# Performance work log

Hardware: AMD Instinct MI355X
Metric: run time of the kernel (lower is better)

The kernel has to match this reference:

```python
import jax, jax.numpy as jnp
import numpy as np

# Blade metric for Cl(1,3) inner product <~A B>_0: sign per basis blade =
# (-1)^{k(k-1)/2} * prod(eta_ii) with eta = diag(1,-1,-1,-1).
# Order: 1 | e0 e1 e2 e3 | e01 e02 e03 e12 e13 e23 | e012 e013 e023 e123 | e0123
BLADE_METRIC = jnp.array(
    [1.0,
     1.0, -1.0, -1.0, -1.0,
     1.0, 1.0, 1.0, -1.0, -1.0, -1.0,
     -1.0, -1.0, -1.0, 1.0,
     -1.0],
    dtype=jnp.float32,
)

B, H, N, MVC, SC = 8, 8, 1024, 8, 32


def setup_inputs() -> dict:
    key = jax.random.key(0)
    ks = jax.random.split(key, 6)
    mv_shape = (B, H, N, MVC, 16)
    s_shape = (B, H, N, SC)
    return {
        "q_mv": jax.random.normal(ks[0], mv_shape, dtype=jnp.float32),
        "k_mv": jax.random.normal(ks[1], mv_shape, dtype=jnp.float32),
        "v_mv": jax.random.normal(ks[2], mv_shape, dtype=jnp.float32),
        "q_s": jax.random.normal(ks[3], s_shape, dtype=jnp.float32),
        "k_s": jax.random.normal(ks[4], s_shape, dtype=jnp.float32),
        "v_s": jax.random.normal(ks[5], s_shape, dtype=jnp.float32),
    }


def reference(q_mv, k_mv, v_mv, q_s, k_s, v_s):
    *lead, n_out, mvc, _ = q_mv.shape
    n_in = k_mv.shape[-3]
    sc = q_s.shape[-1]
    d = 16 * mvc + sc  # total feature dim used for the softmax scale

    # Apply GA blade metric to queries, flatten mv channels, concat scalars.
    qf = jnp.concatenate(
        [(q_mv * BLADE_METRIC).reshape(*lead, n_out, mvc * 16), q_s], axis=-1
    )
    kf = jnp.concatenate([k_mv.reshape(*lead, n_in, mvc * 16), k_s], axis=-1)
    vf = jnp.concatenate([v_mv.reshape(*lead, n_in, mvc * 16), v_s], axis=-1)

    scores = jnp.einsum("bhid,bhjd->bhij", qf, kf) / jnp.sqrt(
        jnp.asarray(d, dtype=qf.dtype)
    )
    attn = jax.nn.softmax(scores, axis=-1)
    out = jnp.einsum("bhij,bhjd->bhid", attn, vf)

    out_mv = out[..., : mvc * 16].reshape(*lead, n_out, mvc, 16)
    out_s = out[..., mvc * 16 :]
    return out_mv, out_s
```

## Files before the change

kernel.cpp:

```cpp
#include <hip/hip_runtime.h>

typedef __attribute__((ext_vector_type(8))) _Float16 f16x8;
typedef __attribute__((ext_vector_type(4))) _Float16 f16x4;
typedef __attribute__((ext_vector_type(4))) float f32x4;

#define BHn 64
#define Nn 1024

static constexpr int kOutMvElems = 8 * 8 * 1024 * 128;
static constexpr float kScaleLog2e = 0.11405506f;
static constexpr unsigned kNegMask = 0xBF1Cu;

__global__ __launch_bounds__(256) void pack_k_kernel(const float* __restrict__ kmv,
                                                     const float* __restrict__ ks,
                                                     _Float16* __restrict__ Kf) {
  int t = blockIdx.x * 256 + threadIdx.x;
  const int total = BHn * Nn * 20;
  if (t >= total) return;
  int row = t / 20, s = t - row * 20;
  const float* src = (s < 16) ? (kmv + (size_t)row * 128 + s * 8)
                              : (ks + (size_t)row * 32 + (s - 16) * 8);
  float4 a = *(const float4*)src;
  float4 b = *(const float4*)(src + 4);
  f16x8 h;
  h[0] = (_Float16)a.x; h[1] = (_Float16)a.y; h[2] = (_Float16)a.z; h[3] = (_Float16)a.w;
  h[4] = (_Float16)b.x; h[5] = (_Float16)b.y; h[6] = (_Float16)b.z; h[7] = (_Float16)b.w;
  *(f16x8*)(Kf + (size_t)row * 160 + s * 8) = h;
}

__global__ __launch_bounds__(256) void pack_vt_kernel(const float* __restrict__ vmv,
                                                      const float* __restrict__ vs,
                                                      _Float16* __restrict__ Vt) {
  __shared__ _Float16 tile[160][72];
  const int bh = blockIdx.y;
  const int kt = blockIdx.x;
  const int tid = threadIdx.x;
  for (int s = tid; s < 64 * 40; s += 256) {
    int key = s / 40, p = s - key * 40;
    int row = bh * Nn + kt * 64 + key;
    const float* src = (p < 32) ? (vmv + (size_t)row * 128 + p * 4)
                                : (vs + (size_t)row * 32 + (p - 32) * 4);
    float4 v = *(const float4*)src;
    int d = p * 4;
    tile[d + 0][key] = (_Float16)v.x;
    tile[d + 1][key] = (_Float16)v.y;
    tile[d + 2][key] = (_Float16)v.z;
    tile[d + 3][key] = (_Float16)v.w;
  }
  __syncthreads();
  for (int s = tid; s < 160 * 8; s += 256) {
    int d = s >> 3, o = s & 7;
    int c32 = (o >> 2) * 32;
    int g4 = (o & 3) * 4;
    f16x4 lo = *(const f16x4*)&tile[d][c32 + g4];
    f16x4 hi = *(const f16x4*)&tile[d][c32 + 16 + g4];
    f16x8 h;
    h[0] = lo[0]; h[1] = lo[1]; h[2] = lo[2]; h[3] = lo[3];
    h[4] = hi[0]; h[5] = hi[1]; h[6] = hi[2]; h[7] = hi[3];
    *(f16x8*)(Vt + ((size_t)(bh * 160 + d)) * 1024 + kt * 64 + o * 8) = h;
  }
}

__global__ __launch_bounds__(512, 2) void geo_attn_kernel(const float* __restrict__ qmv,
                                                          const float* __restrict__ qs,
                                                          const _Float16* __restrict__ Kf,
                                                          const _Float16* __restrict__ Vt,
                                                          float* __restrict__ out) {
  __shared__ _Float16 k_lds[2][64 * 192];
  __shared__ _Float16 v_lds[2][160 * 64];

  const int b = blockIdx.x;
  const int sw = (b & 7) * 32 + (b >> 3);
  const int qb = sw & 3;
  const int bh = sw >> 2;

  const int tid = threadIdx.x;
  const int w = tid >> 6;
  const int l = tid & 63;
  const int g = l >> 4;
  const int nn = l & 15;
  const int swz = (nn & 7) << 3;

  f16x8 qf[2][5];
#pragma unroll
  for (int q2 = 0; q2 < 2; ++q2) {
    const size_t qbase = (size_t)(bh * Nn + qb * 256 + w * 32 + q2 * 16 + nn);
#pragma unroll
    for (int c = 0; c < 5; ++c) {
      const float* src = (c < 4) ? (qmv + qbase * 128 + c * 32 + 8 * g)
                                 : (qs + qbase * 32 + 8 * g);
      float4 a = *(const float4*)src;
      float4 bb = *(const float4*)(src + 4);
      float x[8] = {a.x, a.y, a.z, a.w, bb.x, bb.y, bb.z, bb.w};
#pragma unroll
      for (int i = 0; i < 8; ++i) {
        float v = x[i] * kScaleLog2e;
        if (c < 4) {
          int idx = ((g & 1) << 3) + i;
          v = ((kNegMask >> idx) & 1u) ? -v : v;
        }
        qf[q2][c][i] = (_Float16)v;
      }
    }
  }

  f32x4 acc[2][10];
#pragma unroll
  for (int q2 = 0; q2 < 2; ++q2)
#pragma unroll
    for (int j = 0; j < 10; ++j) acc[q2][j] = (f32x4){0.f, 0.f, 0.f, 0.f};
  float Ma = -3.0e38f, Mb = -3.0e38f, La = 0.f, Lb = 0.f;

  const _Float16* kgbase = Kf + (size_t)(bh * Nn) * 160;
  const _Float16* vgbase = Vt + (size_t)bh * 160 * Nn;

  f16x8 st[5];
  auto stage_load = [&](int key0) {
#pragma unroll
    for (int i = 0; i < 5; ++i) {
      int s = tid + 512 * i;
      if (s < 1280) {
        st[i] = *(const f16x8*)(kgbase + (size_t)key0 * 160 + s * 8);
      } else {
        int s2 = s - 1280;
        int d = s2 >> 3, cs = s2 & 7;
        st[i] = *(const f16x8*)(vgbase + (size_t)d * Nn + key0 + cs * 8);
      }
    }
  };
  auto stage_write = [&](int buf) {
#pragma unroll
    for (int i = 0; i < 5; ++i) {
      int s = tid + 512 * i;
      if (s < 1280) {
        int key = s / 20, p = s - key * 20;
        int idx = (key * 192 + p * 8) ^ ((key & 7) << 3);
        *(f16x8*)&k_lds[buf][idx] = st[i];
      } else {
        int s2 = s - 1280;
        int d = s2 >> 3, cs = s2 & 7;
        int idx = (d * 64 + cs * 8) ^ ((d & 7) << 3);
        *(f16x8*)&v_lds[buf][idx] = st[i];
      }
    }
  };

  stage_load(0);
  stage_write(0);
  __syncthreads();

  for (int it = 0; it < 16; ++it) {
    const int cur = it & 1;
    if (it < 15) stage_load((it + 1) * 64);

    f32x4 sa[4], sb[4];
#pragma unroll
    for (int kb = 0; kb < 4; ++kb) {
      sa[kb] = (f32x4){0.f, 0.f, 0.f, 0.f};
      sb[kb] = (f32x4){0.f, 0.f, 0.f, 0.f};
    }
    __builtin_amdgcn_s_setprio(1);
#pragma unroll
    for (int c = 0; c < 5; ++c) {
      f16x8 kf[4];
#pragma unroll
      for (int kb = 0; kb < 4; ++kb)
        kf[kb] = *(const f16x8*)&k_lds[cur][((16 * kb + nn) * 192 + c * 32 + 8 * g) ^ swz];
#pragma unroll
      for (int kb = 0; kb < 4; ++kb) {
        sa[kb] = __builtin_amdgcn_mfma_f32_16x16x32_f16(kf[kb], qf[0][c], sa[kb], 0, 0, 0);
        sb[kb] = __builtin_amdgcn_mfma_f32_16x16x32_f16(kf[kb], qf[1][c], sb[kb], 0, 0, 0);
      }
    }
    __builtin_amdgcn_s_setprio(0);

    float pma = fmaxf(fmaxf(fmaxf(fmaxf(sa[0][0], sa[0][1]), fmaxf(sa[0][2], sa[0][3])),
                            fmaxf(fmaxf(sa[1][0], sa[1][1]), fmaxf(sa[1][2], sa[1][3]))),
                      fmaxf(fmaxf(fmaxf(sa[2][0], sa[2][1]), fmaxf(sa[2][2], sa[2][3])),
                            fmaxf(fmaxf(sa[3][0], sa[3][1]), fmaxf(sa[3][2], sa[3][3]))));
    float pmb = fmaxf(fmaxf(fmaxf(fmaxf(sb[0][0], sb[0][1]), fmaxf(sb[0][2], sb[0][3])),
                            fmaxf(fmaxf(sb[1][0], sb[1][1]), fmaxf(sb[1][2], sb[1][3]))),
                      fmaxf(fmaxf(fmaxf(sb[2][0], sb[2][1]), fmaxf(sb[2][2], sb[2][3])),
                            fmaxf(fmaxf(sb[3][0], sb[3][1]), fmaxf(sb[3][2], sb[3][3]))));
    pma = fmaxf(pma, __shfl_xor(pma, 16));
    pma = fmaxf(pma, __shfl_xor(pma, 32));
    pmb = fmaxf(pmb, __shfl_xor(pmb, 16));
    pmb = fmaxf(pmb, __shfl_xor(pmb, 32));

    float fsa_l = 1.f, fsb_l = 1.f;
    bool defer = (pma - Ma <= 8.f) && (pmb - Mb <= 8.f);
    if (!__all((int)defer)) {
      float nMa = fmaxf(Ma, pma); fsa_l = exp2f(Ma - nMa); Ma = nMa;
      float nMb = fmaxf(Mb, pmb); fsb_l = exp2f(Mb - nMb); Mb = nMb;
      float fa[4], fb[4];
#pragma unroll
      for (int r = 0; r < 4; ++r) {
        fa[r] = __shfl(fsa_l, 4 * g + r, 16);
        fb[r] = __shfl(fsb_l, 4 * g + r, 16);
      }
#pragma unroll
      for (int j = 0; j < 10; ++j)
#pragma unroll
        for (int r = 0; r < 4; ++r) {
          acc[0][j][r] *= fa[r];
          acc[1][j][r] *= fb[r];
        }
    }

    float rsa = 0.f, rsb = 0.f;
    f16x8 paf[2], pbf[2];
#pragma unroll
    for (int kb = 0; kb < 4; ++kb) {
      const int ch = kb >> 1, off = (kb & 1) * 4;
#pragma unroll
      for (int r = 0; r < 4; ++r) {
        float pa_ = exp2f(sa[kb][r] - Ma);
        float pb_ = exp2f(sb[kb][r] - Mb);
        rsa += pa_; rsb += pb_;
        paf[ch][off + r] = (_Float16)pa_;
        pbf[ch][off + r] = (_Float16)pb_;
      }
    }
    rsa += __shfl_xor(rsa, 16); rsa += __shfl_xor(rsa, 32);
    rsb += __shfl_xor(rsb, 16); rsb += __shfl_xor(rsb, 32);
    La = La * fsa_l + rsa;
    Lb = Lb * fsb_l + rsb;

    __builtin_amdgcn_s_setprio(1);
#pragma unroll
    for (int ch = 0; ch < 2; ++ch) {
#pragma unroll
      for (int j = 0; j < 10; ++j) {
        f16x8 vb = *(const f16x8*)&v_lds[cur][((16 * j + nn) * 64 + ch * 32 + 8 * g) ^ swz];
        acc[0][j] = __builtin_amdgcn_mfma_f32_16x16x32_f16(paf[ch], vb, acc[0][j], 0, 0, 0);
        acc[1][j] = __builtin_amdgcn_mfma_f32_16x16x32_f16(pbf[ch], vb, acc[1][j], 0, 0, 0);
      }
    }
    __builtin_amdgcn_s_setprio(0);

    if (it < 15) stage_write(cur ^ 1);
    __syncthreads();
  }

  float ria = 1.f / La, rib = 1.f / Lb;
  float ra[4], rb_[4];
#pragma unroll
  for (int r = 0; r < 4; ++r) {
    ra[r] = __shfl(ria, 4 * g + r, 16);
    rb_[r] = __shfl(rib, 4 * g + r, 16);
  }
  const int row0 = bh * Nn + qb * 256 + w * 32;
#pragma unroll
  for (int j = 0; j < 10; ++j) {
    const int d = 16 * j + nn;
#pragma unroll
    for (int r = 0; r < 4; ++r) {
      float v0 = acc[0][j][r] * ra[r];
      float v1 = acc[1][j][r] * rb_[r];
      const int r0 = row0 + 4 * g + r;
      const int r1 = row0 + 16 + 4 * g + r;
      if (d < 128) {
        out[(size_t)r0 * 128 + d] = v0;
        out[(size_t)r1 * 128 + d] = v1;
      } else {
        out[(size_t)kOutMvElems + (size_t)r0 * 32 + (d - 128)] = v0;
        out[(size_t)kOutMvElems + (size_t)r1 * 32 + (d - 128)] = v1;
      }
    }
  }
}

extern "C" void kernel_launch(void* const* d_in, const int* in_sizes, int n_in,
                              void* d_out, int out_size, void* d_ws, size_t ws_size,
                              hipStream_t stream) {
  const float* qmv = (const float*)d_in[0];
  const float* kmv = (const float*)d_in[1];
  const float* vmv = (const float*)d_in[2];
  const float* qs = (const float*)d_in[3];
  const float* ks = (const float*)d_in[4];
  const float* vs = (const float*)d_in[5];
  float* out = (float*)d_out;

  _Float16* Kf = (_Float16*)d_ws;
  _Float16* Vt = Kf + (size_t)BHn * Nn * 160;

  pack_k_kernel<<<dim3((BHn * Nn * 20) / 256), dim3(256), 0, stream>>>(kmv, ks, Kf);
  pack_vt_kernel<<<dim3(16, BHn), dim3(256), 0, stream>>>(vmv, vs, Vt);
  geo_attn_kernel<<<dim3(256), dim3(512), 0, stream>>>(qmv, qs, Kf, Vt, out);
}
```

Measured before the change: 94.14 us.

## Use 256-thread blocks with single-buffered LDS and deferred row-sum reduction

Halves the block to 4 waves (128 query rows), doubles the grid to 512 blocks, and drops LDS double-buffering in favour of a single buffer behind two barriers per tile. The per-thread global and LDS staging offsets are precomputed once. The max cross-lane shuffle now runs only when a rescale is needed, and the row-sum shuffle reduction moves out of the loop to the end. The aim is more blocks per CU and fewer shuffles per iteration, at the cost of an extra barrier per tile and K/V being reloaded by twice as many blocks.

```diff
diff --git a/kernel.cpp b/kernel.cpp
--- a/kernel.cpp
+++ b/kernel.cpp
@@ -61,18 +61,18 @@
   }
 }
 
-__global__ __launch_bounds__(512, 2) void geo_attn_kernel(const float* __restrict__ qmv,
+__global__ __launch_bounds__(256, 2) void geo_attn_kernel(const float* __restrict__ qmv,
                                                           const float* __restrict__ qs,
                                                           const _Float16* __restrict__ Kf,
                                                           const _Float16* __restrict__ Vt,
                                                           float* __restrict__ out) {
-  __shared__ _Float16 k_lds[2][64 * 192];
-  __shared__ _Float16 v_lds[2][160 * 64];
+  __shared__ _Float16 k_lds[64 * 192];
+  __shared__ _Float16 v_lds[160 * 64];
 
   const int b = blockIdx.x;
-  const int sw = (b & 7) * 32 + (b >> 3);
-  const int qb = sw & 3;
-  const int bh = sw >> 2;
+  const int sw = (b & 7) * 64 + (b >> 3);
+  const int qb = sw & 7;
+  const int bh = sw >> 3;
 
   const int tid = threadIdx.x;
   const int w = tid >> 6;
@@ -81,10 +81,22 @@
   const int nn = l & 15;
   const int swz = (nn & 7) << 3;
 
+  int gK[5], lKi[5], gV[5], lVi[5];
+#pragma unroll
+  for (int i = 0; i < 5; ++i) {
+    int sk = tid + 256 * i;
+    int key = sk / 20, p = sk - key * 20;
+    gK[i] = key * 160 + p * 8;
+    lKi[i] = (key * 192 + p * 8) ^ ((key & 7) << 3);
+    int d = sk >> 3, cs = sk & 7;
+    gV[i] = d * Nn + cs * 8;
+    lVi[i] = (d * 64 + cs * 8) ^ ((d & 7) << 3);
+  }
+
   f16x8 qf[2][5];
 #pragma unroll
   for (int q2 = 0; q2 < 2; ++q2) {
-    const size_t qbase = (size_t)(bh * Nn + qb * 256 + w * 32 + q2 * 16 + nn);
+    const size_t qbase = (size_t)(bh * Nn + qb * 128 + w * 32 + q2 * 16 + nn);
 #pragma unroll
     for (int c = 0; c < 5; ++c) {
       const float* src = (c < 4) ? (qmv + qbase * 128 + c * 32 + 8 * g)
@@ -111,47 +123,28 @@
     for (int j = 0; j < 10; ++j) acc[q2][j] = (f32x4){0.f, 0.f, 0.f, 0.f};
   float Ma = -3.0e38f, Mb = -3.0e38f, La = 0.f, Lb = 0.f;
 
-  const _Float16* kgbase = Kf + (size_t)(bh * Nn) * 160;
-  const _Float16* vgbase = Vt + (size_t)bh * 160 * Nn;
-
-  f16x8 st[5];
-  auto stage_load = [&](int key0) {
-#pragma unroll
-    for (int i = 0; i < 5; ++i) {
-      int s = tid + 512 * i;
-      if (s < 1280) {
-        st[i] = *(const f16x8*)(kgbase + (size_t)key0 * 160 + s * 8);
-      } else {
-        int s2 = s - 1280;
-        int d = s2 >> 3, cs = s2 & 7;
-        st[i] = *(const f16x8*)(vgbase + (size_t)d * Nn + key0 + cs * 8);
-      }
-    }
-  };
-  auto stage_write = [&](int buf) {
-#pragma unroll
-    for (int i = 0; i < 5; ++i) {
-      int s = tid + 512 * i;
-      if (s < 1280) {
-        int key = s / 20, p = s - key * 20;
-        int idx = (key * 192 + p * 8) ^ ((key & 7) << 3);
-        *(f16x8*)&k_lds[buf][idx] = st[i];
-      } else {
-        int s2 = s - 1280;
-        int d = s2 >> 3, cs = s2 & 7;
-        int idx = (d * 64 + cs * 8) ^ ((d & 7) << 3);
-        *(f16x8*)&v_lds[buf][idx] = st[i];
-      }
-    }
-  };
-
-  stage_load(0);
-  stage_write(0);
+  const _Float16* kg = Kf + (size_t)(bh * Nn) * 160;
+  const _Float16* vg = Vt + (size_t)bh * 160 * Nn;
+
+  f16x8 st[10];
+#pragma unroll
+  for (int i = 0; i < 5; ++i) st[i] = *(const f16x8*)(kg + gK[i]);
+#pragma unroll
+  for (int i = 0; i < 5; ++i) st[5 + i] = *(const f16x8*)(vg + gV[i]);
+#pragma unroll
+  for (int i = 0; i < 5; ++i) *(f16x8*)&k_lds[lKi[i]] = st[i];
+#pragma unroll
+  for (int i = 0; i < 5; ++i) *(f16x8*)&v_lds[lVi[i]] = st[5 + i];
   __syncthreads();
 
   for (int it = 0; it < 16; ++it) {
-    const int cur = it & 1;
-    if (it < 15) stage_load((it + 1) * 64);
+    if (it < 15) {
+      const int key0 = (it + 1) * 64;
+#pragma unroll
+      for (int i = 0; i < 5; ++i) st[i] = *(const f16x8*)(kg + (size_t)key0 * 160 + gK[i]);
+#pragma unroll
+      for (int i = 0; i < 5; ++i) st[5 + i] = *(const f16x8*)(vg + key0 + gV[i]);
+    }
 
     f32x4 sa[4], sb[4];
 #pragma unroll
@@ -165,7 +158,7 @@
       f16x8 kf[4];
 #pragma unroll
       for (int kb = 0; kb < 4; ++kb)
-        kf[kb] = *(const f16x8*)&k_lds[cur][((16 * kb + nn) * 192 + c * 32 + 8 * g) ^ swz];
+        kf[kb] = *(const f16x8*)&k_lds[((16 * kb + nn) * 192 + c * 32 + 8 * g) ^ swz];
 #pragma unroll
       for (int kb = 0; kb < 4; ++kb) {
         sa[kb] = __builtin_amdgcn_mfma_f32_16x16x32_f16(kf[kb], qf[0][c], sa[kb], 0, 0, 0);
@@ -174,29 +167,28 @@
     }
     __builtin_amdgcn_s_setprio(0);
 
-    float pma = fmaxf(fmaxf(fmaxf(fmaxf(sa[0][0], sa[0][1]), fmaxf(sa[0][2], sa[0][3])),
+    float lma = fmaxf(fmaxf(fmaxf(fmaxf(sa[0][0], sa[0][1]), fmaxf(sa[0][2], sa[0][3])),
                             fmaxf(fmaxf(sa[1][0], sa[1][1]), fmaxf(sa[1][2], sa[1][3]))),
                       fmaxf(fmaxf(fmaxf(sa[2][0], sa[2][1]), fmaxf(sa[2][2], sa[2][3])),
                             fmaxf(fmaxf(sa[3][0], sa[3][1]), fmaxf(sa[3][2], sa[3][3]))));
-    float pmb = fmaxf(fmaxf(fmaxf(fmaxf(sb[0][0], sb[0][1]), fmaxf(sb[0][2], sb[0][3])),
+    float lmb = fmaxf(fmaxf(fmaxf(fmaxf(sb[0][0], sb[0][1]), fmaxf(sb[0][2], sb[0][3])),
                             fmaxf(fmaxf(sb[1][0], sb[1][1]), fmaxf(sb[1][2], sb[1][3]))),
                       fmaxf(fmaxf(fmaxf(sb[2][0], sb[2][1]), fmaxf(sb[2][2], sb[2][3])),
                             fmaxf(fmaxf(sb[3][0], sb[3][1]), fmaxf(sb[3][2], sb[3][3]))));
-    pma = fmaxf(pma, __shfl_xor(pma, 16));
-    pma = fmaxf(pma, __shfl_xor(pma, 32));
-    pmb = fmaxf(pmb, __shfl_xor(pmb, 16));
-    pmb = fmaxf(pmb, __shfl_xor(pmb, 32));
-
-    float fsa_l = 1.f, fsb_l = 1.f;
-    bool defer = (pma - Ma <= 8.f) && (pmb - Mb <= 8.f);
-    if (!__all((int)defer)) {
-      float nMa = fmaxf(Ma, pma); fsa_l = exp2f(Ma - nMa); Ma = nMa;
-      float nMb = fmaxf(Mb, pmb); fsb_l = exp2f(Mb - nMb); Mb = nMb;
+    bool need = (lma - Ma > 8.f) || (lmb - Mb > 8.f);
+    if (__any((int)need)) {
+      float pma = fmaxf(lma, __shfl_xor(lma, 16));
+      pma = fmaxf(pma, __shfl_xor(pma, 32));
+      float pmb = fmaxf(lmb, __shfl_xor(lmb, 16));
+      pmb = fmaxf(pmb, __shfl_xor(pmb, 32));
+      float nMa = fmaxf(Ma, pma); float fsa = exp2f(Ma - nMa); Ma = nMa;
+      float nMb = fmaxf(Mb, pmb); float fsb = exp2f(Mb - nMb); Mb = nMb;
+      La *= fsa; Lb *= fsb;
       float fa[4], fb[4];
 #pragma unroll
       for (int r = 0; r < 4; ++r) {
-        fa[r] = __shfl(fsa_l, 4 * g + r, 16);
-        fb[r] = __shfl(fsb_l, 4 * g + r, 16);
+        fa[r] = __shfl(fsa, 4 * g + r, 16);
+        fb[r] = __shfl(fsb, 4 * g + r, 16);
       }
 #pragma unroll
       for (int j = 0; j < 10; ++j)
@@ -221,27 +213,33 @@
         pbf[ch][off + r] = (_Float16)pb_;
       }
     }
-    rsa += __shfl_xor(rsa, 16); rsa += __shfl_xor(rsa, 32);
-    rsb += __shfl_xor(rsb, 16); rsb += __shfl_xor(rsb, 32);
-    La = La * fsa_l + rsa;
-    Lb = Lb * fsb_l + rsb;
+    La += rsa;
+    Lb += rsb;
 
     __builtin_amdgcn_s_setprio(1);
 #pragma unroll
     for (int ch = 0; ch < 2; ++ch) {
 #pragma unroll
       for (int j = 0; j < 10; ++j) {
-        f16x8 vb = *(const f16x8*)&v_lds[cur][((16 * j + nn) * 64 + ch * 32 + 8 * g) ^ swz];
+        f16x8 vb = *(const f16x8*)&v_lds[((16 * j + nn) * 64 + ch * 32 + 8 * g) ^ swz];
         acc[0][j] = __builtin_amdgcn_mfma_f32_16x16x32_f16(paf[ch], vb, acc[0][j], 0, 0, 0);
         acc[1][j] = __builtin_amdgcn_mfma_f32_16x16x32_f16(pbf[ch], vb, acc[1][j], 0, 0, 0);
       }
     }
     __builtin_amdgcn_s_setprio(0);
 
-    if (it < 15) stage_write(cur ^ 1);
-    __syncthreads();
-  }
-
+    if (it < 15) {
+      __syncthreads();
+#pragma unroll
+      for (int i = 0; i < 5; ++i) *(f16x8*)&k_lds[lKi[i]] = st[i];
+#pragma unroll
+      for (int i = 0; i < 5; ++i) *(f16x8*)&v_lds[lVi[i]] = st[5 + i];
+      __syncthreads();
+    }
+  }
+
+  La += __shfl_xor(La, 16); La += __shfl_xor(La, 32);
+  Lb += __shfl_xor(Lb, 16); Lb += __shfl_xor(Lb, 32);
   float ria = 1.f / La, rib = 1.f / Lb;
   float ra[4], rb_[4];
 #pragma unroll
@@ -249,7 +247,7 @@
     ra[r] = __shfl(ria, 4 * g + r, 16);
     rb_[r] = __shfl(rib, 4 * g + r, 16);
   }
-  const int row0 = bh * Nn + qb * 256 + w * 32;
+  const int row0 = bh * Nn + qb * 128 + w * 32;
 #pragma unroll
   for (int j = 0; j < 10; ++j) {
     const int d = 16 * j + nn;
@@ -286,5 +284,5 @@
 
   pack_k_kernel<<<dim3((BHn * Nn * 20) / 256), dim3(256), 0, stream>>>(kmv, ks, Kf);
   pack_vt_kernel<<<dim3(16, BHn), dim3(256), 0, stream>>>(vmv, vs, Vt);
-  geo_attn_kernel<<<dim3(256), dim3(512), 0, stream>>>(qmv, qs, Kf, Vt, out);
-}
+  geo_attn_kernel<<<dim3(512), dim3(256), 0, stream>>>(qmv, qs, Kf, Vt, out);
+}
```

Measured after the change: 120.6 us. 28.1% more time.
